# Performance work log

Hardware: AMD Instinct MI355X
Metric: run time of the kernel (lower is better)

## Reference

```python
import jax, jax.numpy as jnp
from jax import lax
import numpy as np

SEQ_LEN = 96; PRED_LEN = 96; SIGNAL_LEN = 16; NUM_NODES = 256
EMBED = 128; HIDDEN = 64; K_NN = 8; S_SCALE = 2.0; CHEB_ORDER = 2
MA_K = 3; BATCH = 16
C_FREQ = SIGNAL_LEN // 2 + 1          # 9 rfft bins
M_NODES = NUM_NODES * C_FREQ          # nodes per sample graph


def _sin_posemb(pos, dim):
    half = dim // 2
    freqs = 1.0 / (10000.0 ** (np.arange(half) / half))
    ang = pos[:, None] * freqs[None, :]
    return np.concatenate([np.sin(ang), np.cos(ang)], axis=-1).astype(np.float32)


def setup_inputs():
    key = jax.random.key(0)
    ks = jax.random.split(key, 12)
    x = jax.random.normal(ks[0], (BATCH, SEQ_LEN, NUM_NODES), jnp.float32)
    # Chebyshev (order 2) approx of Haar framelet filters cos(xi/2), sin(xi/2) on [0, pi]
    t = np.linspace(-1.0, 1.0, 201); xi = (t + 1.0) * np.pi / 2.0
    ch = np.polynomial.chebyshev
    approx = np.stack([ch.chebfit(t, np.cos(xi / 2.0), CHEB_ORDER),
                       ch.chebfit(t, np.sin(xi / 2.0), CHEB_ORDER)]).astype(np.float32)
    freq_emb = _sin_posemb(np.arange(C_FREQ, dtype=np.float32) * S_SCALE, EMBED)
    sc = (2.0 / EMBED) ** 0.5
    return dict(
        x=x,
        approx=jnp.asarray(approx),                 # [F=2, K=3]
        theta=jnp.ones((2,), jnp.float32),
        fr_Wr=jax.random.normal(ks[1], (EMBED, EMBED), jnp.float32) * sc,
        fr_Wi=jax.random.normal(ks[2], (EMBED, EMBED), jnp.float32) * sc,
        eo_Wr=jax.random.normal(ks[3], (1, EMBED), jnp.float32) * sc,
        eo_Wi=jax.random.normal(ks[4], (1, EMBED), jnp.float32) * sc,
        freq_emb=jnp.asarray(freq_emb),             # [C, EMBED]
        n1_w=jnp.ones((NUM_NODES,), jnp.float32), n1_b=jnp.zeros((NUM_NODES,), jnp.float32),
        n2_w=jnp.ones((NUM_NODES,), jnp.float32), n2_b=jnp.zeros((NUM_NODES,), jnp.float32),
        W1_w=jax.random.normal(ks[5], (HIDDEN, SEQ_LEN), jnp.float32) * (1.0 / SEQ_LEN ** 0.5),
        W1_b=jnp.zeros((HIDDEN,), jnp.float32),
        W2_w=jax.random.normal(ks[6], (HIDDEN, HIDDEN), jnp.float32) * (1.0 / HIDDEN ** 0.5),
        W2_b=jnp.zeros((HIDDEN,), jnp.float32),
        Wt_w=jax.random.normal(ks[7], (HIDDEN, SEQ_LEN), jnp.float32) * (1.0 / SEQ_LEN ** 0.5),
        Wt_b=jnp.zeros((HIDDEN,), jnp.float32),
        W3_w=jax.random.normal(ks[8], (PRED_LEN, HIDDEN), jnp.float32) * (1.0 / HIDDEN ** 0.5),
        W3_b=jnp.zeros((PRED_LEN,), jnp.float32),
    )


def _clinear(z, Wr, Wi):
    xr, xi = z.real, z.imag
    return lax.complex(xr @ Wr.T - xi @ Wi.T, xr @ Wi.T + xi @ Wr.T)


def _csilu(z):
    return lax.complex(jax.nn.silu(z.real), jax.nn.silu(z.imag))


def _cheb_prop(h, row, col, ew, coeffs):
    # Chebyshev recurrence with A_norm(h) = scatter_add(row, (ew/s) * h[col])
    w = (ew / S_SCALE)[:, None]
    def A(hh):
        return jnp.zeros_like(hh).at[row].add(w * hh[col])
    Tx0 = h
    out = coeffs[0] * Tx0
    Tx1 = -A(Tx0)
    out = out + coeffs[1] * Tx1
    for ki in range(2, CHEB_ORDER + 1):
        Tx2 = -2.0 * A(Tx1) - Tx0
        out = out + coeffs[ki] * Tx2
        Tx0, Tx1 = Tx1, Tx2
    return out


def _knn_one(feat):
    # feat [M, 2] -> symmetrised degree-normalised KNN edges
    sq = jnp.sum(feat * feat, axis=1)
    d2 = sq[:, None] + sq[None, :] - 2.0 * (feat @ feat.T)
    d2 = jnp.where(jnp.eye(M_NODES, dtype=bool), jnp.inf, d2)
    idx = lax.top_k(-d2, K_NN)[1]                      # smallest distances
    src = jnp.repeat(jnp.arange(M_NODES), K_NN)
    dst = idx.reshape(-1)
    r = jnp.concatenate([src, dst])
    c = jnp.concatenate([dst, src])
    deg = jnp.zeros((M_NODES,), jnp.float32).at[r].add(1.0)
    dinv = (deg + 1e-8) ** -0.5
    return r, c, dinv[r] * dinv[c]


def _moving_avg(x):
    pad = MA_K // 2
    front = jnp.repeat(x[:, :1, :], pad, axis=1)
    back = jnp.repeat(x[:, -1:, :], MA_K - 1 - pad, axis=1)
    xp = jnp.concatenate([front, x, back], axis=1)     # (B, T+k-1, N)
    cs = jnp.cumsum(xp, axis=1)
    cs = jnp.concatenate([jnp.zeros_like(cs[:, :1, :]), cs], axis=1)
    return (cs[:, MA_K:, :] - cs[:, :-MA_K, :]) / MA_K  # (B, T, N)


def _inorm(h, w, b):
    mu = jnp.mean(h, axis=-1, keepdims=True)
    var = jnp.mean((h - mu) ** 2, axis=-1, keepdims=True)
    return (h - mu) / jnp.sqrt(var + 1e-5) * w[None, :, None] + b[None, :, None]


def _forward(x, approx, theta, fr_Wr, fr_Wi, eo_Wr, eo_Wi, freq_emb,
             n1_w, n1_b, n2_w, n2_b, W1_w, W1_b, W2_w, W2_b, Wt_w, Wt_b, W3_w, W3_b):
    B, T, N = x.shape
    trend = _moving_avg(x)
    seasonal = x - trend
    S = jnp.fft.rfft(seasonal, n=SIGNAL_LEN, axis=1, norm='ortho')   # (B, C, N) c64
    S_perm = jnp.transpose(S, (0, 2, 1))                             # (B, N, C)
    node_feat = S_perm[..., None] * freq_emb                         # (B, N, C, E) c64
    batch_x = node_feat.reshape(B * M_NODES, EMBED)
    sg = S_perm.reshape(B, M_NODES)
    feat = lax.stop_gradient(jnp.stack([sg.real, sg.imag], axis=-1))  # (B, M, 2)
    rs, cs_, ews = jax.vmap(_knn_one)(feat)
    off = (jnp.arange(B) * M_NODES)[:, None]
    row = (rs + off).reshape(-1)
    col = (cs_ + off).reshape(-1)
    ew = ews.reshape(-1)
    # framelet layer: sum of F filtered Chebyshev propagations
    acc = jnp.zeros_like(batch_x)
    for i in range(approx.shape[0]):
        acc = acc + theta[i] * _cheb_prop(batch_x, row, col, ew, approx[i])
    h = _csilu(_clinear(acc, fr_Wr, fr_Wi))
    S_out = _clinear(h, eo_Wr, eo_Wi).reshape(B, N, C_FREQ)
    H = jnp.fft.irfft(jnp.transpose(S_out, (0, 2, 1)), n=SEQ_LEN, axis=1, norm='ortho')
    H = jnp.transpose(H, (0, 2, 1))                                  # (B, N, T)
    H = jax.nn.silu(_inorm(H, n1_w, n1_b))
    H = H @ W1_w.T + W1_b
    H = jax.nn.silu(_inorm(H, n2_w, n2_b))
    H = H @ W2_w.T + W2_b
    trend_emb = jnp.transpose(trend, (0, 2, 1)) @ Wt_w.T + Wt_b
    return (H + trend_emb) @ W3_w.T + W3_b                           # (B, N, pred_len)


def reference(x, approx, theta, fr_Wr, fr_Wi, eo_Wr, eo_Wi, freq_emb,
              n1_w, n1_b, n2_w, n2_b, W1_w, W1_b, W2_w, W2_b, Wt_w, Wt_b, W3_w, W3_b):
    return _forward(x, approx, theta, fr_Wr, fr_Wi, eo_Wr, eo_Wi, freq_emb,
                    n1_w, n1_b, n2_w, n2_b, W1_w, W1_b, W2_w, W2_b, Wt_w, Wt_b, W3_w, W3_b)
```

## Files before the change

### kernel.cpp

```cpp
#include <hip/hip_runtime.h>
#include <math.h>
#include <float.h>

#define BATCH 16
#define SEQ 96
#define NNODE 256
#define CFREQ 9
#define MNODE (NNODE * CFREQ)
#define BM (BATCH * MNODE)
#define KNN 8
#define EMBED 128
#define HIDDEN 64
#define TN (SEQ * NNODE)
#define KCAP 64
#define NBLK (BM / 256)
#define HROWS 16
#define FEW (CFREQ * EMBED)

__constant__ float COS16[16] = {
    1.0f, 0.9238795325112867f, 0.7071067811865476f, 0.3826834323650898f,
    0.0f, -0.3826834323650898f, -0.7071067811865476f, -0.9238795325112867f,
    -1.0f, -0.9238795325112867f, -0.7071067811865476f, -0.3826834323650898f,
    0.0f, 0.3826834323650898f, 0.7071067811865476f, 0.9238795325112867f};
__constant__ float SIN16[16] = {
    0.0f, 0.3826834323650898f, 0.7071067811865476f, 0.9238795325112867f,
    1.0f, 0.9238795325112867f, 0.7071067811865476f, 0.3826834323650898f,
    0.0f, -0.3826834323650898f, -0.7071067811865476f, -0.9238795325112867f,
    -1.0f, -0.9238795325112867f, -0.7071067811865476f, -0.3826834323650898f};

static __device__ __forceinline__ float silu_f(float x) {
    return x / (1.0f + expf(-x));
}

static __device__ __forceinline__ float rank_h(float2 fj, float xi2, float yi2) {
    float sqj = __fmaf_rn(fj.y, fj.y, __fmul_rn(fj.x, fj.x));
    return __fmaf_rn(xi2, fj.x, __fmaf_rn(yi2, fj.y, sqj));
}

__global__ void __launch_bounds__(256) prep_kernel(
    const float* __restrict__ x, float* __restrict__ S, int* __restrict__ cnt,
    const float* __restrict__ femb, const float* __restrict__ Wr,
    const float* __restrict__ Wi, float* __restrict__ FE, int* __restrict__ gtotal) {
    int gid = blockIdx.x * 256 + threadIdx.x;
    if (gid < BM) {
        if (gid == 0) *gtotal = 0;
        cnt[gid] = 0;
        int b = gid / MNODE;
        int m = gid - b * MNODE;
        int n = m / CFREQ;
        int c = m - n * CFREQ;
        const float* xb = x + b * TN + n;
        float xv[17];
        #pragma unroll
        for (int t = 0; t < 17; ++t) xv[t] = xb[t * NNODE];
        float re = 0.0f, im = 0.0f;
        #pragma unroll
        for (int t = 0; t < 16; ++t) {
            int tm = t > 0 ? t - 1 : 0;
            float tr = (xv[tm] + xv[t] + xv[t + 1]) * (1.0f / 3.0f);
            float s = xv[t] - tr;
            int k = (c * t) & 15;
            re += s * COS16[k];
            im -= s * SIN16[k];
        }
        S[gid * 2 + 0] = re * 0.25f;
        S[gid * 2 + 1] = im * 0.25f;
    } else {
        int f = gid - BM;
        if (f < FEW) {
            int c = f / EMBED;
            int e = f - c * EMBED;
            float ar = 0.0f, ai = 0.0f;
            for (int k = 0; k < EMBED; ++k) {
                float fv = femb[c * EMBED + k];
                ar += fv * Wr[e * EMBED + k];
                ai += fv * Wi[e * EMBED + k];
            }
            FE[f * 2 + 0] = ar;
            FE[f * 2 + 1] = ai;
        }
    }
}

__global__ void __launch_bounds__(256, 8) knn_kernel(const float* __restrict__ S,
                                                     int* __restrict__ idx, int* __restrict__ cnt) {
    __shared__ float2 f[MNODE];
    __shared__ unsigned long long kbuf[4][KCAP];
    int b = blockIdx.y;
    int tid = threadIdx.x;
    for (int t = tid; t < MNODE; t += 256) {
        f[t] = make_float2(S[(b * MNODE + t) * 2 + 0], S[(b * MNODE + t) * 2 + 1]);
    }
    __syncthreads();
    int wave = tid >> 6, lane = tid & 63;
    int i = blockIdx.x * 4 + wave;
    float2 fi = f[i];
    float xi2 = __fmul_rn(-2.0f, fi.x), yi2 = __fmul_rn(-2.0f, fi.y);
    int lane_i = __builtin_amdgcn_readfirstlane(i & 63);
    int k_i    = __builtin_amdgcn_readfirstlane(i >> 6);

    float h[36];
    float mymin = FLT_MAX;
    #pragma unroll
    for (int k = 0; k < 36; ++k) {
        int j = lane + (k << 6);
        float hh = rank_h(f[j], xi2, yi2);
        if (k == k_i && lane == lane_i) hh = FLT_MAX;
        h[k] = hh;
        mymin = fminf(mymin, hh);
    }
    float g = mymin;
    g = fminf(g, __shfl_xor(g, 1, 64));
    g = fminf(g, __shfl_xor(g, 2, 64));
    g = fminf(g, __shfl_xor(g, 4, 64));
    float T = g;
    T = fmaxf(T, __shfl_xor(T, 8, 64));
    T = fmaxf(T, __shfl_xor(T, 16, 64));
    T = fmaxf(T, __shfl_xor(T, 32, 64));
    unsigned long long* mybuf = kbuf[wave];
    const unsigned long long lmask = (1ull << lane) - 1ull;
    int total = 0;
    #pragma unroll
    for (int k = 0; k < 36; ++k) {
        bool pred = h[k] <= T;
        unsigned long long mask = __ballot(pred);
        if (pred) {
            int pos = total + (int)__popcll(mask & lmask);
            if (pos < KCAP) {
                unsigned int bits = __float_as_uint(h[k]);
                if (bits == 0x80000000u) bits = 0u;
                unsigned int s = bits ^ (unsigned int)(((int)bits >> 31) | 0x80000000);
                mybuf[pos] = ((unsigned long long)s << 32) | (unsigned int)(lane + (k << 6));
            }
        }
        total += (int)__popcll(mask);
    }

    if (total >= KNN && total <= KCAP) {
        int padded = (total + 7) & ~7;
        if (lane < padded - total) mybuf[total + lane] = ~0ull;
        for (int p = lane; p < total; p += 64) {
            unsigned long long mykey = mybuf[p];
            int rank = 0;
            for (int q = 0; q < padded; q += 8) {
                const ulonglong2* bp = (const ulonglong2*)&mybuf[q];
                ulonglong2 a = bp[0], b2 = bp[1], c2 = bp[2], d2 = bp[3];
                rank += (int)(a.x  < mykey) + (int)(a.y  < mykey)
                      + (int)(b2.x < mykey) + (int)(b2.y < mykey)
                      + (int)(c2.x < mykey) + (int)(c2.y < mykey)
                      + (int)(d2.x < mykey) + (int)(d2.y < mykey);
            }
            if (rank < KNN) {
                int j = (int)(unsigned int)(mykey & 0xFFFFFFFFull);
                idx[(b * MNODE + i) * KNN + rank] = j;
                atomicAdd(&cnt[b * MNODE + j], 1);
            }
        }
    } else {
        const unsigned long long SENT = ~0ull;
        unsigned long long k0 = SENT, k1 = SENT, k2 = SENT, k3 = SENT,
                           k4 = SENT, k5 = SENT, k6 = SENT, k7 = SENT;
        #pragma unroll
        for (int k = 0; k < 36; ++k) {
            unsigned int bits = __float_as_uint(h[k]);
            if (bits == 0x80000000u) bits = 0u;
            unsigned int s = bits ^ (unsigned int)(((int)bits >> 31) | 0x80000000);
            unsigned long long key = ((unsigned long long)s << 32) | (unsigned int)(lane + (k << 6));
            if (key < k7) {
                k7 = key;
                if (k7 < k6) { unsigned long long t = k6; k6 = k7; k7 = t; }
                if (k6 < k5) { unsigned long long t = k5; k5 = k6; k6 = t; }
                if (k5 < k4) { unsigned long long t = k4; k4 = k5; k5 = t; }
                if (k4 < k3) { unsigned long long t = k3; k3 = k4; k4 = t; }
                if (k3 < k2) { unsigned long long t = k2; k2 = k3; k3 = t; }
                if (k2 < k1) { unsigned long long t = k1; k1 = k2; k2 = t; }
                if (k1 < k0) { unsigned long long t = k0; k0 = k1; k1 = t; }
            }
        }
        unsigned long long mywin = 0;
        #pragma unroll
        for (int r = 0; r < KNN; ++r) {
            unsigned long long hh = k0;
            #pragma unroll
            for (int off = 32; off > 0; off >>= 1) {
                unsigned long long o = __shfl_xor(hh, off, 64);
                if (o < hh) hh = o;
            }
            if (lane == r) mywin = hh;
            if (k0 == hh) {
                k0 = k1; k1 = k2; k2 = k3; k3 = k4; k4 = k5; k5 = k6; k6 = k7; k7 = SENT;
            }
        }
        if (lane < KNN) {
            int j = (int)(unsigned int)(mywin & 0xFFFFFFFFull);
            idx[(b * MNODE + i) * KNN + lane] = j;
            atomicAdd(&cnt[b * MNODE + j], 1);
        }
    }
}

__global__ void __launch_bounds__(256) scan_kernel(
    const int* __restrict__ cnt, const float* __restrict__ S,
    float* __restrict__ dinv, float* __restrict__ PS,
    int* __restrict__ gtotal, int2* __restrict__ oc, int* __restrict__ fptr) {
    __shared__ int wsum[4];
    __shared__ int sbase;
    int tid = threadIdx.x;
    int lane = tid & 63, wv = tid >> 6;
    int gid = blockIdx.x * 256 + tid;
    int v = cnt[gid];
    float deg = (float)(KNN + v);
    float dv = 1.0f / sqrtf(deg + 1e-8f);
    dinv[gid] = dv;
    PS[gid * 2 + 0] = dv * S[gid * 2 + 0];
    PS[gid * 2 + 1] = dv * S[gid * 2 + 1];
    int x = v;
    #pragma unroll
    for (int off = 1; off < 64; off <<= 1) {
        int y = __shfl_up(x, off, 64);
        if (lane >= off) x += y;
    }
    if (lane == 63) wsum[wv] = x;
    __syncthreads();
    if (tid == 0) sbase = atomicAdd(gtotal, wsum[0] + wsum[1] + wsum[2] + wsum[3]);
    __syncthreads();
    int base = sbase;
    for (int w = 0; w < wv; ++w) base += wsum[w];
    int o = base + x - v;
    oc[gid] = make_int2(o, v);
    fptr[gid] = o;
}

__global__ void fill_kernel(const int* __restrict__ idx,
                            int* __restrict__ fptr, int* __restrict__ rev) {
    int gid = blockIdx.x * blockDim.x + threadIdx.x;
    if (gid >= BM * KNN) return;
    int b = gid / (MNODE * KNN);
    int rem = gid - b * (MNODE * KNN);
    int i = rem / KNN;
    int gj = b * MNODE + idx[gid];
    int pos = atomicAdd(&fptr[gj], 1);
    rev[pos] = b * MNODE + i;
}

__global__ void __launch_bounds__(256) gather1_kernel(
    const int* __restrict__ idx, const int2* __restrict__ oc,
    const int* __restrict__ rev, const float* __restrict__ dinv, const float* __restrict__ PS,
    float* __restrict__ zA, float* __restrict__ zAw) {
    int gid = blockIdx.x * blockDim.x + threadIdx.x;
    if (gid >= BM * CFREQ) return;
    int gi = gid / CFREQ;
    int c = gid - gi * CFREQ;
    int b = gi / MNODE;
    float ax = 0.0f, ay = 0.0f;
    #pragma unroll
    for (int k = 0; k < KNN; ++k) {
        int gj = b * MNODE + idx[gi * KNN + k];
        bool m = (gj % CFREQ) == c;
        float2 p = ((const float2*)PS)[gj];
        ax += m ? p.x : 0.0f;
        ay += m ? p.y : 0.0f;
    }
    int2 ocv = oc[gi];
    int o = ocv.x, e = o + ocv.y;
    for (int p_ = o; p_ < e; ++p_) {
        int gk = rev[p_];
        bool m = (gk % CFREQ) == c;
        float2 p = ((const float2*)PS)[gk];
        ax += m ? p.x : 0.0f;
        ay += m ? p.y : 0.0f;
    }
    float dv = dinv[gi];
    float s = dv * 0.5f;
    float zx = s * ax, zy = s * ay;
    zA[gid * 2 + 0] = zx;
    zA[gid * 2 + 1] = zy;
    zAw[gid * 2 + 0] = dv * zx;
    zAw[gid * 2 + 1] = dv * zy;
}

__global__ void __launch_bounds__(256) gather2_kernel(
    const int* __restrict__ idx, const int2* __restrict__ oc,
    const int* __restrict__ rev, const float* __restrict__ dinv,
    const float* __restrict__ zA, const float* __restrict__ zAw,
    const float* __restrict__ theta, const float* __restrict__ approx,
    float* __restrict__ zF) {
    int gid = blockIdx.x * blockDim.x + threadIdx.x;
    if (gid >= BM * CFREQ) return;
    float a1 = theta[0] * approx[1] + theta[1] * approx[4];
    float a2 = theta[0] * approx[2] + theta[1] * approx[5];
    float cb = -a1, cc = 2.0f * a2;
    int gi = gid / CFREQ;
    int c = gid - gi * CFREQ;
    int b = gi / MNODE;
    float ax = 0.0f, ay = 0.0f;
    #pragma unroll
    for (int k = 0; k < KNN; ++k) {
        int gj = b * MNODE + idx[gi * KNN + k];
        float2 v = ((const float2*)zAw)[gj * CFREQ + c];
        ax += v.x;
        ay += v.y;
    }
    int2 ocv = oc[gi];
    int o = ocv.x, e = o + ocv.y;
    for (int p = o; p < e; ++p) {
        int gk = rev[p];
        float2 v = ((const float2*)zAw)[gk * CFREQ + c];
        ax += v.x;
        ay += v.y;
    }
    float s = dinv[gi] * 0.5f;
    float2 za = ((const float2*)zA)[gid];
    zF[gid * 2 + 0] = cb * za.x + cc * (s * ax);
    zF[gid * 2 + 1] = cb * za.y + cc * (s * ay);
}

__global__ void __launch_bounds__(256) rowproj_kernel(
    const float* __restrict__ S, const float* __restrict__ zF,
    const float* __restrict__ FE, const float* __restrict__ eoWr, const float* __restrict__ eoWi,
    const float* __restrict__ theta, const float* __restrict__ approx,
    float* __restrict__ Sout) {
    int wave = threadIdx.x >> 6;
    int lane = threadIdx.x & 63;
    int r = blockIdx.x * 4 + wave;
    if (r >= BM) return;
    float a0 = theta[0] * approx[0] + theta[1] * approx[3];
    float a2 = theta[0] * approx[2] + theta[1] * approx[5];
    float ca = a0 - a2;
    int cr = r % CFREQ;
    float sr = S[r * 2 + 0], si = S[r * 2 + 1];
    int e1 = lane + 64;
    float ur0 = 0.0f, ui0 = 0.0f, ur1 = 0.0f, ui1 = 0.0f;
    #pragma unroll
    for (int c = 0; c < CFREQ; ++c) {
        float2 zf = ((const float2*)zF)[r * CFREQ + c];
        float zr = zf.x, zi = zf.y;
        if (c == cr) { zr += ca * sr; zi += ca * si; }
        float fr0 = FE[(c * EMBED + lane) * 2 + 0], fi0 = FE[(c * EMBED + lane) * 2 + 1];
        float fr1 = FE[(c * EMBED + e1) * 2 + 0],  fi1 = FE[(c * EMBED + e1) * 2 + 1];
        ur0 += zr * fr0 - zi * fi0;  ui0 += zr * fi0 + zi * fr0;
        ur1 += zr * fr1 - zi * fi1;  ui1 += zr * fi1 + zi * fr1;
    }
    float hr0 = silu_f(ur0), hi0 = silu_f(ui0);
    float hr1 = silu_f(ur1), hi1 = silu_f(ui1);
    float wr0 = eoWr[lane], wi0 = eoWi[lane], wr1 = eoWr[e1], wi1 = eoWi[e1];
    float p = hr0 * wr0 - hi0 * wi0 + hr1 * wr1 - hi1 * wi1;
    float q = hr0 * wi0 + hi0 * wr0 + hr1 * wi1 + hi1 * wr1;
    #pragma unroll
    for (int off = 32; off > 0; off >>= 1) {
        p += __shfl_down(p, off, 64);
        q += __shfl_down(q, off, 64);
    }
    if (lane == 0) {
        Sout[r * 2 + 0] = p;
        Sout[r * 2 + 1] = q;
    }
}

__global__ void __launch_bounds__(1024) head_kernel(
    const float* __restrict__ Sout, const float* __restrict__ x,
    const float* __restrict__ n1w, const float* __restrict__ n1b,
    const float* __restrict__ n2w, const float* __restrict__ n2b,
    const float* __restrict__ W1w, const float* __restrict__ W1b,
    const float* __restrict__ W2w, const float* __restrict__ W2b,
    const float* __restrict__ Wtw, const float* __restrict__ Wtb,
    const float* __restrict__ W3w, const float* __restrict__ W3b,
    float* __restrict__ out) {
    __shared__ float tabc[96], tabs[96];
    __shared__ float srow[HROWS][18];
    __shared__ float tbuf[HROWS][96];
    __shared__ float hraw[HROWS][96];
    __shared__ float sH[HROWS][96];
    __shared__ float h2[HROWS][64];
    __shared__ float s3[HROWS][64];
    __shared__ float red[HROWS][2];
    __shared__ float wbuf[6240];
    int tid = threadIdx.x;
    int wave = tid >> 6, lane = tid & 63;
    int bn0 = blockIdx.x * HROWS;
    if (tid < 96) {
        double a = 6.283185307179586476925286766559 * (double)tid / 96.0;
        tabc[tid] = (float)cos(a);
        tabs[tid] = (float)sin(a);
    }
    for (int i = tid; i < HROWS * 96; i += 1024) {
        int g = i / 96, t = i - g * 96;
        int bn = bn0 + g;
        hraw[g][t] = x[(bn >> 8) * TN + t * NNODE + (bn & 255)];
    }
    if (tid < HROWS * 18) {
        int g = tid / 18, k = tid - g * 18;
        srow[g][k] = Sout[(bn0 + g) * 18 + k];
    }
    __syncthreads();
    for (int i = tid; i < HROWS * 96; i += 1024) {
        int g = i / 96, t = i - g * 96;
        int tm = t > 0 ? t - 1 : 0;
        int tp = t < SEQ - 1 ? t + 1 : SEQ - 1;
        tbuf[g][t] = (hraw[g][tm] + hraw[g][t] + hraw[g][tp]) * (1.0f / 3.0f);
    }
    __syncthreads();
    for (int i = tid; i < HROWS * 96; i += 1024) {
        int g = i / 96, t = i - g * 96;
        float acc = srow[g][0];
        #pragma unroll
        for (int c = 1; c < CFREQ; ++c) {
            int k = (c * t) % 96;
            acc += 2.0f * (srow[g][2 * c] * tabc[k] - srow[g][2 * c + 1] * tabs[k]);
        }
        hraw[g][t] = acc * 0.10206207261596575f;
    }
    __syncthreads();
    {
        float v = hraw[wave][lane] + ((lane < 32) ? hraw[wave][64 + lane] : 0.0f);
        #pragma unroll
        for (int off = 32; off > 0; off >>= 1) v += __shfl_down(v, off, 64);
        if (lane == 0) red[wave][0] = v * (1.0f / 96.0f);
    }
    __syncthreads();
    {
        float mu = red[wave][0];
        float d0 = hraw[wave][lane] - mu;
        float v = d0 * d0;
        if (lane < 32) { float d1 = hraw[wave][64 + lane] - mu; v += d1 * d1; }
        #pragma unroll
        for (int off = 32; off > 0; off >>= 1) v += __shfl_down(v, off, 64);
        if (lane == 0) red[wave][1] = v * (1.0f / 96.0f);
    }
    __syncthreads();
    for (int i = tid; i < HROWS * 96; i += 1024) {
        int g = i / 96, t = i - g * 96;
        int n = (bn0 + g) & 255;
        float xn = (hraw[g][t] - red[g][0]) / sqrtf(red[g][1] + 1e-5f) * n1w[n] + n1b[n];
        sH[g][t] = silu_f(xn);
    }
    for (int i = tid; i < HIDDEN * 96; i += 1024) {
        int rr = i / 96;
        wbuf[rr * 97 + (i - rr * 96)] = W1w[i];
    }
    __syncthreads();
    float v1;
    {
        float acc = W1b[lane];
        #pragma unroll 8
        for (int t = 0; t < 96; ++t) acc += sH[wave][t] * wbuf[lane * 97 + t];
        v1 = acc;
    }
    {
        float s = v1;
        #pragma unroll
        for (int off = 32; off > 0; off >>= 1) s += __shfl_down(s, off, 64);
        s = __shfl(s, 0, 64);
        float mu2 = s * (1.0f / 64.0f);
        float d = v1 - mu2;
        float vs = d * d;
        #pragma unroll
        for (int off = 32; off > 0; off >>= 1) vs += __shfl_down(vs, off, 64);
        vs = __shfl(vs, 0, 64);
        float var2 = vs * (1.0f / 64.0f);
        int n = (bn0 + wave) & 255;
        float xn = (v1 - mu2) / sqrtf(var2 + 1e-5f) * n2w[n] + n2b[n];
        h2[wave][lane] = silu_f(xn);
    }
    __syncthreads();
    for (int i = tid; i < HIDDEN * HIDDEN; i += 1024) {
        wbuf[(i >> 6) * 65 + (i & 63)] = W2w[i];
    }
    __syncthreads();
    float v3;
    {
        float acc = W2b[lane];
        #pragma unroll 8
        for (int h = 0; h < 64; ++h) acc += h2[wave][h] * wbuf[lane * 65 + h];
        v3 = acc;
    }
    __syncthreads();
    for (int i = tid; i < HIDDEN * 96; i += 1024) {
        int rr = i / 96;
        wbuf[rr * 97 + (i - rr * 96)] = Wtw[i];
    }
    __syncthreads();
    {
        float acc = Wtb[lane];
        #pragma unroll 8
        for (int t = 0; t < 96; ++t) acc += tbuf[wave][t] * wbuf[lane * 97 + t];
        s3[wave][lane] = v3 + acc;
    }
    __syncthreads();
    for (int i = tid; i < 96 * HIDDEN; i += 1024) {
        wbuf[(i >> 6) * 65 + (i & 63)] = W3w[i];
    }
    __syncthreads();
    for (int i = tid; i < HROWS * 96; i += 1024) {
        int g = i / 96, t = i - g * 96;
        float acc = W3b[t];
        #pragma unroll 8
        for (int h = 0; h < 64; ++h) acc += s3[g][h] * wbuf[t * 65 + h];
        out[(bn0 + g) * 96 + t] = acc;
    }
}

extern "C" void kernel_launch(void* const* d_in, const int* in_sizes, int n_in,
                              void* d_out, int out_size, void* d_ws, size_t ws_size,
                              hipStream_t stream) {
    const float* x     = (const float*)d_in[0];
    const float* approx= (const float*)d_in[1];
    const float* theta = (const float*)d_in[2];
    const float* frWr  = (const float*)d_in[3];
    const float* frWi  = (const float*)d_in[4];
    const float* eoWr  = (const float*)d_in[5];
    const float* eoWi  = (const float*)d_in[6];
    const float* femb  = (const float*)d_in[7];
    const float* n1w   = (const float*)d_in[8];
    const float* n1b   = (const float*)d_in[9];
    const float* n2w   = (const float*)d_in[10];
    const float* n2b   = (const float*)d_in[11];
    const float* W1w   = (const float*)d_in[12];
    const float* W1b   = (const float*)d_in[13];
    const float* W2w   = (const float*)d_in[14];
    const float* W2b   = (const float*)d_in[15];
    const float* Wtw   = (const float*)d_in[16];
    const float* Wtb   = (const float*)d_in[17];
    const float* W3w   = (const float*)d_in[18];
    const float* W3b   = (const float*)d_in[19];
    float* out = (float*)d_out;

    char* ws = (char*)d_ws;
    size_t off = 0;
    auto alloc = [&](size_t bytes) -> void* {
        void* p = ws + off;
        off = (off + bytes + 255) & ~(size_t)255;
        return p;
    };
    float* S     = (float*)alloc((size_t)BM * 2 * 4);
    int*   idx   = (int*)  alloc((size_t)BM * KNN * 4);
    float* dinv  = (float*)alloc((size_t)BM * 4);
    float* PS    = (float*)alloc((size_t)BM * 2 * 4);
    float* FE    = (float*)alloc((size_t)FEW * 2 * 4);
    float* Sout  = (float*)alloc((size_t)BM * 2 * 4);
    int2*  oc    = (int2*) alloc((size_t)BM * 8);
    int*   rev   = (int*)  alloc((size_t)BM * KNN * 4);
    float* zA    = (float*)alloc((size_t)BM * CFREQ * 2 * 4);
    float* zAw   = (float*)alloc((size_t)BM * CFREQ * 2 * 4);
    float* zF    = (float*)alloc((size_t)BM * CFREQ * 2 * 4);
    int*   cnt   = (int*)  alloc((size_t)BM * 4);
    int*   fptr  = (int*)  alloc((size_t)BM * 4);
    int*   gtotal= (int*)  alloc(256);

    prep_kernel<<<(BM + FEW + 255) / 256, 256, 0, stream>>>(x, S, cnt, femb, frWr, frWi, FE, gtotal);
    knn_kernel<<<dim3(MNODE / 4, BATCH), 256, 0, stream>>>(S, idx, cnt);
    scan_kernel<<<NBLK, 256, 0, stream>>>(cnt, S, dinv, PS, gtotal, oc, fptr);
    fill_kernel<<<(BM * KNN + 255) / 256, 256, 0, stream>>>(idx, fptr, rev);
    gather1_kernel<<<(BM * CFREQ + 255) / 256, 256, 0, stream>>>(idx, oc, rev, dinv, PS, zA, zAw);
    gather2_kernel<<<(BM * CFREQ + 255) / 256, 256, 0, stream>>>(idx, oc, rev, dinv, zA, zAw,
                                                                 theta, approx, zF);
    rowproj_kernel<<<BM / 4, 256, 0, stream>>>(S, zF, FE, eoWr, eoWi, theta, approx, Sout);
    head_kernel<<<BATCH * NNODE / HROWS, 1024, 0, stream>>>(Sout, x, n1w, n1b, n2w, n2b,
                                                            W1w, W1b, W2w, W2b, Wtw, Wtb, W3w, W3b, out);
}
```

Measured before the change: 243.2 us.

## Fuse second graph gather into the row projection kernel

Merges the second Chebyshev gather into the per-row projection kernel. Each wave's first 36 lanes compute the nine frequency gathers for its row, split four ways over neighbours and reduced with shuffles, then stage the results in LDS for the projection. This drops the zF intermediate buffer round-trip through global memory and one kernel launch. In exchange, gather latency now sits in front of the projection inside each wave. The LDS handoff relies on wave-level ordering with no explicit barrier.

```diff
diff --git a/kernel.cpp b/kernel.cpp
--- a/kernel.cpp
+++ b/kernel.cpp
@@ -279,61 +279,58 @@
     zAw[gid * 2 + 1] = dv * zy;
 }
 
-__global__ void __launch_bounds__(256) gather2_kernel(
+__global__ void __launch_bounds__(256) g2proj_kernel(
     const int* __restrict__ idx, const int2* __restrict__ oc,
     const int* __restrict__ rev, const float* __restrict__ dinv,
     const float* __restrict__ zA, const float* __restrict__ zAw,
-    const float* __restrict__ theta, const float* __restrict__ approx,
-    float* __restrict__ zF) {
-    int gid = blockIdx.x * blockDim.x + threadIdx.x;
-    if (gid >= BM * CFREQ) return;
-    float a1 = theta[0] * approx[1] + theta[1] * approx[4];
-    float a2 = theta[0] * approx[2] + theta[1] * approx[5];
-    float cb = -a1, cc = 2.0f * a2;
-    int gi = gid / CFREQ;
-    int c = gid - gi * CFREQ;
-    int b = gi / MNODE;
-    float ax = 0.0f, ay = 0.0f;
-    #pragma unroll
-    for (int k = 0; k < KNN; ++k) {
-        int gj = b * MNODE + idx[gi * KNN + k];
-        float2 v = ((const float2*)zAw)[gj * CFREQ + c];
-        ax += v.x;
-        ay += v.y;
-    }
-    int2 ocv = oc[gi];
-    int o = ocv.x, e = o + ocv.y;
-    for (int p = o; p < e; ++p) {
-        int gk = rev[p];
-        float2 v = ((const float2*)zAw)[gk * CFREQ + c];
-        ax += v.x;
-        ay += v.y;
-    }
-    float s = dinv[gi] * 0.5f;
-    float2 za = ((const float2*)zA)[gid];
-    zF[gid * 2 + 0] = cb * za.x + cc * (s * ax);
-    zF[gid * 2 + 1] = cb * za.y + cc * (s * ay);
-}
-
-__global__ void __launch_bounds__(256) rowproj_kernel(
-    const float* __restrict__ S, const float* __restrict__ zF,
-    const float* __restrict__ FE, const float* __restrict__ eoWr, const float* __restrict__ eoWi,
+    const float* __restrict__ S, const float* __restrict__ FE,
+    const float* __restrict__ eoWr, const float* __restrict__ eoWi,
     const float* __restrict__ theta, const float* __restrict__ approx,
     float* __restrict__ Sout) {
+    __shared__ float2 zfb[4][CFREQ];
     int wave = threadIdx.x >> 6;
     int lane = threadIdx.x & 63;
     int r = blockIdx.x * 4 + wave;
     if (r >= BM) return;
     float a0 = theta[0] * approx[0] + theta[1] * approx[3];
+    float a1 = theta[0] * approx[1] + theta[1] * approx[4];
     float a2 = theta[0] * approx[2] + theta[1] * approx[5];
-    float ca = a0 - a2;
+    float ca = a0 - a2, cb = -a1, cc = 2.0f * a2;
+    int b = r / MNODE;
+    int2 ocv = oc[r];
+    if (lane < 36) {
+        int c = lane >> 2, sub = lane & 3;
+        float ax = 0.0f, ay = 0.0f;
+        #pragma unroll
+        for (int k = sub; k < KNN; k += 4) {
+            int gj = b * MNODE + idx[r * KNN + k];
+            float2 v = ((const float2*)zAw)[gj * CFREQ + c];
+            ax += v.x;
+            ay += v.y;
+        }
+        int o = ocv.x, e = o + ocv.y;
+        for (int p = o + sub; p < e; p += 4) {
+            int gk = rev[p];
+            float2 v = ((const float2*)zAw)[gk * CFREQ + c];
+            ax += v.x;
+            ay += v.y;
+        }
+        ax += __shfl_xor(ax, 1, 64);  ay += __shfl_xor(ay, 1, 64);
+        ax += __shfl_xor(ax, 2, 64);  ay += __shfl_xor(ay, 2, 64);
+        if (sub == 0) {
+            float s = dinv[r] * 0.5f;
+            float2 za = ((const float2*)zA)[r * CFREQ + c];
+            zfb[wave][c] = make_float2(cb * za.x + cc * (s * ax),
+                                       cb * za.y + cc * (s * ay));
+        }
+    }
     int cr = r % CFREQ;
     float sr = S[r * 2 + 0], si = S[r * 2 + 1];
     int e1 = lane + 64;
     float ur0 = 0.0f, ui0 = 0.0f, ur1 = 0.0f, ui1 = 0.0f;
     #pragma unroll
     for (int c = 0; c < CFREQ; ++c) {
-        float2 zf = ((const float2*)zF)[r * CFREQ + c];
+        float2 zf = zfb[wave][c];
         float zr = zf.x, zi = zf.y;
         if (c == cr) { zr += ca * sr; zi += ca * si; }
         float fr0 = FE[(c * EMBED + lane) * 2 + 0], fi0 = FE[(c * EMBED + lane) * 2 + 1];
@@ -542,7 +539,6 @@
     int*   rev   = (int*)  alloc((size_t)BM * KNN * 4);
     float* zA    = (float*)alloc((size_t)BM * CFREQ * 2 * 4);
     float* zAw   = (float*)alloc((size_t)BM * CFREQ * 2 * 4);
-    float* zF    = (float*)alloc((size_t)BM * CFREQ * 2 * 4);
     int*   cnt   = (int*)  alloc((size_t)BM * 4);
     int*   fptr  = (int*)  alloc((size_t)BM * 4);
     int*   gtotal= (int*)  alloc(256);
@@ -552,9 +548,8 @@
     scan_kernel<<<NBLK, 256, 0, stream>>>(cnt, S, dinv, PS, gtotal, oc, fptr);
     fill_kernel<<<(BM * KNN + 255) / 256, 256, 0, stream>>>(idx, fptr, rev);
     gather1_kernel<<<(BM * CFREQ + 255) / 256, 256, 0, stream>>>(idx, oc, rev, dinv, PS, zA, zAw);
-    gather2_kernel<<<(BM * CFREQ + 255) / 256, 256, 0, stream>>>(idx, oc, rev, dinv, zA, zAw,
-                                                                 theta, approx, zF);
-    rowproj_kernel<<<BM / 4, 256, 0, stream>>>(S, zF, FE, eoWr, eoWi, theta, approx, Sout);
+    g2proj_kernel<<<BM / 4, 256, 0, stream>>>(idx, oc, rev, dinv, zA, zAw, S, FE,
+                                              eoWr, eoWi, theta, approx, Sout);
     head_kernel<<<BATCH * NNODE / HROWS, 1024, 0, stream>>>(Sout, x, n1w, n1b, n2w, n2b,
                                                             W1w, W1b, W2w, W2b, Wtw, Wtb, W3w, W3b, out);
 }
```

Result: no change. 239.0 us (-1.7%).
